# Kernel tuning notes

Hardware: AMD Instinct MI355X
Metric: run time of the kernel (lower is better)

## Reference

```python
import jax, jax.numpy as jnp
import numpy as np

N, E, G = 100000, 1600000, 2000
D_IN, D_H, D_MLP, D_OUT = 768, 128, 32, 2


def setup_inputs() -> dict:
    key = jax.random.key(0)
    ks = jax.random.split(key, 12)
    x = jax.random.normal(ks[0], (N, D_IN), dtype=jnp.float32)
    edge_index = jax.random.randint(ks[1], (2, E), 0, N, dtype=jnp.int64)
    edge_attr = jax.random.uniform(ks[2], (E, 1), dtype=jnp.float32)
    batch = jnp.sort(jax.random.randint(ks[3], (N,), 0, G, dtype=jnp.int64))
    s1 = 1.0 / np.sqrt(D_IN)
    s2 = 1.0 / np.sqrt(D_H)
    s3 = 1.0 / np.sqrt(D_MLP)
    return {
        "x": x, "edge_index": edge_index, "edge_attr": edge_attr,
        "batch": batch, "num_graphs": G,
        "W1i": jax.random.normal(ks[4], (D_IN, D_H), dtype=jnp.float32) * s1,
        "W1r": jax.random.normal(ks[5], (D_IN, D_H), dtype=jnp.float32) * s1,
        "b1": jnp.zeros((D_H,), dtype=jnp.float32),
        "W2i": jax.random.normal(ks[6], (D_H, D_H), dtype=jnp.float32) * s2,
        "W2r": jax.random.normal(ks[7], (D_H, D_H), dtype=jnp.float32) * s2,
        "b2": jnp.zeros((D_H,), dtype=jnp.float32),
        "Wl1": jax.random.normal(ks[8], (D_H, D_MLP), dtype=jnp.float32) * s2,
        "bl1": jnp.zeros((D_MLP,), dtype=jnp.float32),
        "Wl2": jax.random.normal(ks[9], (D_MLP, D_OUT), dtype=jnp.float32) * s3,
        "bl2": jnp.zeros((D_OUT,), dtype=jnp.float32),
    }


def _arma_conv(x, row, col, ew, Wi, Wr, b, n_nodes):
    # gcn_norm without self-loops: D^{-1/2} A D^{-1/2}
    deg = jax.ops.segment_sum(ew, col, num_segments=n_nodes)
    dinv = jnp.where(deg > 0, jax.lax.rsqrt(jnp.where(deg > 0, deg, 1.0)), 0.0)
    norm = dinv[row] * ew * dinv[col]
    h = x @ Wi                                   # [N, F_out]
    msg = h[row] * norm[:, None]                 # gather + scale  [E, F_out]
    agg = jax.ops.segment_sum(msg, col, num_segments=n_nodes)
    return jax.nn.relu(agg + x @ Wr + b)         # ARMA: K=1, T=1, act=ReLU


def reference(x, edge_index, edge_attr, batch, num_graphs,
              W1i, W1r, b1, W2i, W2r, b2, Wl1, bl1, Wl2, bl2):
    row, col = edge_index[0], edge_index[1]
    ew = edge_attr.reshape(-1)
    n = x.shape[0]
    h = jax.nn.elu(_arma_conv(x, row, col, ew, W1i, W1r, b1, n))
    node_x = _arma_conv(h, row, col, ew, W2i, W2r, b2, n)
    # global mean pool over graphs
    sums = jax.ops.segment_sum(node_x, batch, num_segments=num_graphs)
    cnt = jax.ops.segment_sum(jnp.ones((n,), node_x.dtype), batch, num_segments=num_graphs)
    graph_x = sums / jnp.maximum(cnt, 1.0)[:, None]
    pred = jax.nn.elu(graph_x @ Wl1 + bl1) @ Wl2 + bl2
    return pred
```

## Files before the change

### kernel.cpp

```cpp
#include <hip/hip_runtime.h>
#include <hip/hip_bf16.h>
#include <math.h>

typedef __attribute__((ext_vector_type(8))) short short8;
typedef __attribute__((ext_vector_type(4))) float f32x4;
typedef __attribute__((ext_vector_type(2))) float f32x2;
typedef __attribute__((address_space(1))) const void gvoid;
typedef __attribute__((address_space(3))) void lvoid;

#define NC 8

__device__ __forceinline__ unsigned short f2bf(float f) {
    unsigned int u = __builtin_bit_cast(unsigned int, f);
    return (unsigned short)((u + 0x7fffu + ((u >> 16) & 1u)) >> 16);
}
__device__ __forceinline__ float b2f(short s) {
    return __builtin_bit_cast(float, ((unsigned int)(unsigned short)s) << 16);
}
__device__ __forceinline__ unsigned int cvtpk(float lo, float hi) {
    unsigned int r;
    asm("v_cvt_pk_bf16_f32 %0, %1, %2" : "=v"(r) : "v"(lo), "v"(hi));
    return r;
}
__device__ __forceinline__ unsigned int pk8_lo(float a, float b, unsigned int old) {
    return (unsigned int)__builtin_amdgcn_cvt_pk_fp8_f32(a, b, (int)old, false);
}
__device__ __forceinline__ unsigned int pk8_hi(float a, float b, unsigned int old) {
    return (unsigned int)__builtin_amdgcn_cvt_pk_fp8_f32(a, b, (int)old, true);
}
__device__ __forceinline__ f32x2 up8_lo(unsigned int v) {
    return __builtin_amdgcn_cvt_pk_f32_fp8((int)v, false);
}
__device__ __forceinline__ f32x2 up8_hi(unsigned int v) {
    return __builtin_amdgcn_cvt_pk_f32_fp8((int)v, true);
}
__device__ __forceinline__ void acc16(float* A, const uint4 u, const float n) {
    f32x2 p;
    p = up8_lo(u.x); A[0]  = fmaf(p.x, n, A[0]);  A[1]  = fmaf(p.y, n, A[1]);
    p = up8_hi(u.x); A[2]  = fmaf(p.x, n, A[2]);  A[3]  = fmaf(p.y, n, A[3]);
    p = up8_lo(u.y); A[4]  = fmaf(p.x, n, A[4]);  A[5]  = fmaf(p.y, n, A[5]);
    p = up8_hi(u.y); A[6]  = fmaf(p.x, n, A[6]);  A[7]  = fmaf(p.y, n, A[7]);
    p = up8_lo(u.z); A[8]  = fmaf(p.x, n, A[8]);  A[9]  = fmaf(p.y, n, A[9]);
    p = up8_hi(u.z); A[10] = fmaf(p.x, n, A[10]); A[11] = fmaf(p.y, n, A[11]);
    p = up8_lo(u.w); A[12] = fmaf(p.x, n, A[12]); A[13] = fmaf(p.y, n, A[13]);
    p = up8_hi(u.w); A[14] = fmaf(p.x, n, A[14]); A[15] = fmaf(p.y, n, A[15]);
}

__global__ __launch_bounds__(256) void hist_conv_kernel(
    const int* __restrict__ ei, const float* __restrict__ ea,
    unsigned long long* __restrict__ packed, int* __restrict__ rank, int N, int E,
    int eBlocks,
    const float* __restrict__ W1i, const float* __restrict__ W1r,
    const float* __restrict__ W2i, const float* __restrict__ W2r,
    unsigned short* __restrict__ W1t, unsigned short* __restrict__ W2t)
{
    if ((int)blockIdx.x < eBlocks) {
        int e = blockIdx.x * 256 + threadIdx.x;
        if (e >= E) return;
        const int copy = blockIdx.x & (NC - 1);
        int c = ei[(size_t)E + e];
        unsigned long long fx = (unsigned long long)(ea[e] * 1048576.0f + 0.5f);
        unsigned long long old = atomicAdd(&packed[(size_t)copy * N + c], (1ULL << 42) | fx);
        rank[e] = (int)(old >> 42);
    } else {
        int id = (blockIdx.x - eBlocks) * 256 + threadIdx.x;
        if (id < 256 * 768) {
            int n = id / 768, j = id % 768;
            int k = (j & ~63) | ((((j >> 3) & 7) ^ (n & 7)) << 3) | (j & 7);
            float v = (n < 128) ? W1i[k * 128 + n] : W1r[k * 128 + (n - 128)];
            W1t[id] = f2bf(v);
        } else {
            int id2 = id - 256 * 768;
            if (id2 < 128 * 256) {
                int n = id2 >> 8, j = id2 & 255;
                int k = (j & ~63) | ((((j >> 3) & 7) ^ (n & 7)) << 3) | (j & 7);
                float v = (k < 128) ? W2i[k * 128 + n] : W2r[(k - 128) * 128 + n];
                W2t[id2] = f2bf(v);
            }
        }
    }
}

__global__ __launch_bounds__(256) void scan1p_kernel(
    const unsigned long long* __restrict__ packed, int* __restrict__ out,
    int* __restrict__ blksum, int n)
{
    __shared__ int part[256];
    const int t = threadIdx.x;
    const int base = blockIdx.x * 1024 + t * 4;
    int v[4];
#pragma unroll
    for (int q = 0; q < 4; ++q) {
        int s = 0;
        if (base + q < n) {
#pragma unroll
            for (int p = 0; p < NC; ++p)
                s += (int)(packed[(size_t)p * n + base + q] >> 42);
        }
        v[q] = s;
    }
    const int s = v[0] + v[1] + v[2] + v[3];
    part[t] = s;
    __syncthreads();
    for (int off = 1; off < 256; off <<= 1) {
        int x = (t >= off) ? part[t - off] : 0;
        __syncthreads();
        part[t] += x;
        __syncthreads();
    }
    if (t == 255) blksum[blockIdx.x] = part[255];
    int run = part[t] - s;
#pragma unroll
    for (int q = 0; q < 4; ++q) {
        if (base + q < n) out[base + q] = run;
        run += v[q];
    }
}

__global__ __launch_bounds__(256) void scan3_kernel(
    int* __restrict__ rowptr, const int* __restrict__ blksum,
    int* __restrict__ wpb, const unsigned long long* __restrict__ packed,
    float* __restrict__ dinv, int n, int Etot, int nb)
{
    __shared__ int tmp[256];
    __shared__ int sexcl[256];
    const int t = threadIdx.x;
    const int v = (t < nb) ? blksum[t] : 0;
    tmp[t] = v;
    __syncthreads();
    for (int off = 1; off < 256; off <<= 1) {
        int x = (t >= off) ? tmp[t - off] : 0;
        __syncthreads();
        tmp[t] += x;
        __syncthreads();
    }
    sexcl[t] = tmp[t] - v;
    __syncthreads();
    const int i = blockIdx.x * 256 + t;
    if (i == 0) rowptr[n] = Etot;
    if (i >= n) return;
    int base = rowptr[i] + sexcl[i >> 10];
    rowptr[i] = base;
    unsigned long long degfx = 0;
    int acc = base;
#pragma unroll
    for (int p = 0; p < NC; ++p) {
        unsigned long long vv = packed[(size_t)p * n + i];
        wpb[(size_t)p * n + i] = acc;
        acc += (int)(vv >> 42);
        degfx += vv & ((1ULL << 42) - 1);
    }
    dinv[i] = (degfx > 0) ? rsqrtf((float)degfx * 9.5367431640625e-7f) : 0.f;
}

__global__ __launch_bounds__(512) void gemm1_place_kernel(
    const float* __restrict__ A, const unsigned short* __restrict__ Wt,
    const float* __restrict__ bias, unsigned char* __restrict__ outP8,
    unsigned short* __restrict__ outR, int M, int K, int gB,
    const int* __restrict__ ei, const float* __restrict__ ea,
    const float* __restrict__ dinv, const int* __restrict__ wpb,
    const int* __restrict__ rank, int2* __restrict__ csr, int E)
{
    __shared__ __align__(16) unsigned char As[2][64 * 128];
    __shared__ __align__(16) unsigned char Bs[256 * 128];

    if ((int)blockIdx.x >= gB) {
        int e = (blockIdx.x - gB) * 512 + threadIdx.x;
        if (e >= E) return;
        const int copy = (e >> 8) & (NC - 1);
        int r = ei[e];
        int c = ei[(size_t)E + e];
        float nm = dinv[r] * ea[e] * dinv[c];
        int pos = wpb[(size_t)copy * M + c] + rank[e];
        int2 rec;
        rec.x = r;
        rec.y = __builtin_bit_cast(int, nm);
        csr[pos] = rec;
        return;
    }

    const int t = threadIdx.x;
    const int m0 = blockIdx.x * 64;
    const int lane = t & 63;
    const int wid = t >> 6;
    const int wm = wid >> 2;
    const int wn = wid & 3;
    const int lr = lane & 15;
    const int lk = (lane >> 4) * 8;

    f32x4 acc[2][4] = {};

    const int sr = t >> 3;
    const int sk = (t & 7) * 8;
    const int aRow = m0 + sr;
    const bool aOk = (aRow < M);
    const float* aSrc = A + (size_t)(aOk ? aRow : 0) * K + sk;
    const int aDst = sr * 128 + ((sk * 2) ^ ((sr & 7) << 4));
    const unsigned short* bSrc = Wt + (size_t)(lane >> 3) * K + (lane & 7) * 8;

    const int NIT = K >> 6;

#pragma unroll
    for (int i = 0; i < 4; ++i) {
        const int chunk = i * 8 + wid;
        __builtin_amdgcn_global_load_lds(
            (gvoid*)(bSrc + (size_t)chunk * 8 * K),
            (lvoid*)(Bs + chunk * 1024), 16, 0, 0);
    }
    {
        float4 f0 = {}, f1 = {};
        if (aOk) { f0 = *(const float4*)(aSrc); f1 = *(const float4*)(aSrc + 4); }
        uint4 uv = {cvtpk(f0.x, f0.y), cvtpk(f0.z, f0.w),
                    cvtpk(f1.x, f1.y), cvtpk(f1.z, f1.w)};
        *(uint4*)(&As[0][aDst]) = uv;
    }

    for (int it = 0; it < NIT; ++it) {
        const int cur = it & 1;
        const int nxt = cur ^ 1;
        const bool hasNext = (it + 1 < NIT);
        const int k1 = (it + 1) << 6;

        __syncthreads();

        float4 g0 = {}, g1 = {};
        if (hasNext && aOk) {
            g0 = *(const float4*)(aSrc + k1);
            g1 = *(const float4*)(aSrc + k1 + 4);
        }

#pragma unroll
        for (int ks = 0; ks < 2; ++ks) {
            short8 a[2], b[4];
#pragma unroll
            for (int mf = 0; mf < 2; ++mf) {
                const int r = wm * 32 + mf * 16 + lr;
                a[mf] = *(const short8*)(&As[cur][r * 128 + (((ks * 32 + lk) * 2) ^ ((r & 7) << 4))]);
            }
#pragma unroll
            for (int nf = 0; nf < 4; ++nf) {
                const int n = wn * 64 + nf * 16 + lr;
                b[nf] = *(const short8*)(Bs + n * 128 + (((ks * 32 + lk) * 2) ^ ((n & 7) << 4)));
            }
#pragma unroll
            for (int mf = 0; mf < 2; ++mf)
#pragma unroll
                for (int nf = 0; nf < 4; ++nf)
                    acc[mf][nf] = __builtin_amdgcn_mfma_f32_16x16x32_bf16(
                        a[mf], b[nf], acc[mf][nf], 0, 0, 0);
        }

        if (hasNext) {
            uint4 uv = {cvtpk(g0.x, g0.y), cvtpk(g0.z, g0.w),
                        cvtpk(g1.x, g1.y), cvtpk(g1.z, g1.w)};
            *(uint4*)(&As[nxt][aDst]) = uv;
        }

        __syncthreads();

        if (hasNext) {
#pragma unroll
            for (int i = 0; i < 4; ++i) {
                const int chunk = i * 8 + wid;
                __builtin_amdgcn_global_load_lds(
                    (gvoid*)(bSrc + (size_t)chunk * 8 * K + k1),
                    (lvoid*)(Bs + chunk * 1024), 16, 0, 0);
            }
        }
    }

#pragma unroll
    for (int mf = 0; mf < 2; ++mf) {
#pragma unroll
        for (int nf = 0; nf < 4; ++nf) {
            const int n = wn * 64 + nf * 16 + lr;
            const f32x4 v = acc[mf][nf];
            const int mb = m0 + wm * 32 + mf * 16 + (lane >> 4) * 4;
            if (n < 128) {
                const unsigned int u01 = pk8_lo(v[0], v[1], 0u);
                const unsigned int u23 = pk8_lo(v[2], v[3], 0u);
                if (mb + 0 < M) outP8[(size_t)(mb + 0) * 128 + n] = (unsigned char)(u01);
                if (mb + 1 < M) outP8[(size_t)(mb + 1) * 128 + n] = (unsigned char)(u01 >> 8);
                if (mb + 2 < M) outP8[(size_t)(mb + 2) * 128 + n] = (unsigned char)(u23);
                if (mb + 3 < M) outP8[(size_t)(mb + 3) * 128 + n] = (unsigned char)(u23 >> 8);
            } else {
                const int nl = n - 128;
                const float badd = bias[nl];
#pragma unroll
                for (int j = 0; j < 4; ++j) {
                    if (mb + j < M) outR[(size_t)(mb + j) * 128 + nl] = f2bf(v[j] + badd);
                }
            }
        }
    }
}

__global__ __launch_bounds__(512) void gemm_mfma_single(
    const unsigned short* __restrict__ Aa,
    const unsigned short* __restrict__ Ah,
    const unsigned short* __restrict__ Wt,
    const float* __restrict__ bias,
    unsigned short* __restrict__ outX, int M)
{
    __shared__ __align__(16) unsigned char As[128 * 128];
    __shared__ __align__(16) unsigned char Bs[128 * 128];

    const int t = threadIdx.x;
    const int m0 = blockIdx.x * 128;
    const int lane = t & 63;
    const int wid = t >> 6;
    const int wm = wid >> 1;
    const int wn = wid & 1;
    const int lr = lane & 15;
    const int lk = (lane >> 4) * 8;

    f32x4 acc[2][4] = {};

    const int sr = t >> 2;
    const int sk = (t & 3) * 16;
    const int aRow = m0 + sr;
    const bool aOk = (aRow < M);
    const int rowSafe = aOk ? aRow : 0;
    const int sw = (sr & 7) << 4;
    const unsigned short* bSrc = Wt + (size_t)(lane >> 3) * 256 + (lane & 7) * 8;

    for (int k0 = 0; k0 < 256; k0 += 64) {
#pragma unroll
        for (int i = 0; i < 2; ++i) {
            const int chunk = i * 8 + wid;
            __builtin_amdgcn_global_load_lds(
                (gvoid*)(bSrc + (size_t)chunk * 8 * 256 + k0),
                (lvoid*)(Bs + chunk * 1024), 16, 0, 0);
        }
        const unsigned short* src =
            (k0 < 128 ? Aa : Ah) + (size_t)rowSafe * 128 + (k0 & 127) + sk;
        const short8 v0 = *(const short8*)(src);
        const short8 v1 = *(const short8*)(src + 8);
        *(short8*)(As + sr * 128 + ((sk * 2) ^ sw)) = v0;
        *(short8*)(As + sr * 128 + ((sk * 2 + 16) ^ sw)) = v1;
        __syncthreads();
#pragma unroll
        for (int ks = 0; ks < 2; ++ks) {
            short8 a[2], b[4];
#pragma unroll
            for (int mf = 0; mf < 2; ++mf) {
                const int r = wm * 32 + mf * 16 + lr;
                a[mf] = *(const short8*)(As + r * 128 + (((ks * 32 + lk) * 2) ^ ((r & 7) << 4)));
            }
#pragma unroll
            for (int nf = 0; nf < 4; ++nf) {
                const int n = wn * 64 + nf * 16 + lr;
                b[nf] = *(const short8*)(Bs + n * 128 + (((ks * 32 + lk) * 2) ^ ((n & 7) << 4)));
            }
#pragma unroll
            for (int mf = 0; mf < 2; ++mf)
#pragma unroll
                for (int nf = 0; nf < 4; ++nf)
                    acc[mf][nf] = __builtin_amdgcn_mfma_f32_16x16x32_bf16(
                        a[mf], b[nf], acc[mf][nf], 0, 0, 0);
        }
        __syncthreads();
    }

#pragma unroll
    for (int mf = 0; mf < 2; ++mf) {
#pragma unroll
        for (int nf = 0; nf < 4; ++nf) {
            const int n = wn * 64 + nf * 16 + lr;
            const float bb = bias[n];
            const f32x4 v = acc[mf][nf];
#pragma unroll
            for (int j = 0; j < 4; ++j) {
                const int m = m0 + wm * 32 + mf * 16 + (lane >> 4) * 4 + j;
                if (m < M) outX[(size_t)m * 128 + n] = f2bf(fmaxf(v[j] + bb, 0.f));
            }
        }
    }
}

__global__ __launch_bounds__(256) void agg_bias_relu(
    const unsigned char* __restrict__ P8, const unsigned short* __restrict__ Rbf,
    const int* __restrict__ rowptr, const int2* __restrict__ csr,
    unsigned short* __restrict__ hout, unsigned char* __restrict__ h8out, int N)
{
    const int i = blockIdx.x * 32 + (threadIdx.x >> 3);
    const int l = threadIdx.x & 7;
    if (i >= N) return;
    const int beg = rowptr[i];
    const int end = rowptr[i + 1];
    const int c = l * 16;

    float A0[16] = {}, A1[16] = {};
    int j = beg;
    for (; j + 1 < end; j += 2) {
        const int2 e0 = csr[j], e1 = csr[j + 1];
        const uint4 u0 = *(const uint4*)(P8 + (size_t)e0.x * 128 + c);
        const uint4 u1 = *(const uint4*)(P8 + (size_t)e1.x * 128 + c);
        acc16(A0, u0, __builtin_bit_cast(float, e0.y));
        acc16(A1, u1, __builtin_bit_cast(float, e1.y));
    }
    if (j < end) {
        const int2 e0 = csr[j];
        const uint4 u0 = *(const uint4*)(P8 + (size_t)e0.x * 128 + c);
        acc16(A0, u0, __builtin_bit_cast(float, e0.y));
    }
    const short8 r0 = *(const short8*)(Rbf + (size_t)i * 128 + c);
    const short8 r1 = *(const short8*)(Rbf + (size_t)i * 128 + c + 8);
    float s[16];
    short8 o0, o1;
#pragma unroll
    for (int q = 0; q < 8; ++q) {
        s[q] = fmaxf(A0[q] + A1[q] + b2f(r0[q]), 0.f);
        o0[q] = (short)f2bf(s[q]);
    }
#pragma unroll
    for (int q = 8; q < 16; ++q) {
        s[q] = fmaxf(A0[q] + A1[q] + b2f(r1[q - 8]), 0.f);
        o1[q - 8] = (short)f2bf(s[q]);
    }
    *(short8*)(hout + (size_t)i * 128 + c) = o0;
    *(short8*)(hout + (size_t)i * 128 + c + 8) = o1;
    uint4 w;
    w.x = pk8_hi(s[2],  s[3],  pk8_lo(s[0],  s[1],  0u));
    w.y = pk8_hi(s[6],  s[7],  pk8_lo(s[4],  s[5],  0u));
    w.z = pk8_hi(s[10], s[11], pk8_lo(s[8],  s[9],  0u));
    w.w = pk8_hi(s[14], s[15], pk8_lo(s[12], s[13], 0u));
    *(uint4*)(h8out + (size_t)i * 128 + c) = w;
}

__global__ __launch_bounds__(256) void agg_plain(
    const unsigned char* __restrict__ H8,
    const int* __restrict__ rowptr, const int2* __restrict__ csr,
    unsigned short* __restrict__ ahout, int N)
{
    const int i = blockIdx.x * 32 + (threadIdx.x >> 3);
    const int l = threadIdx.x & 7;
    if (i >= N) return;
    const int beg = rowptr[i];
    const int end = rowptr[i + 1];
    const int c = l * 16;

    float A0[16] = {}, A1[16] = {};
    int j = beg;
    for (; j + 1 < end; j += 2) {
        const int2 e0 = csr[j], e1 = csr[j + 1];
        const uint4 u0 = *(const uint4*)(H8 + (size_t)e0.x * 128 + c);
        const uint4 u1 = *(const uint4*)(H8 + (size_t)e1.x * 128 + c);
        acc16(A0, u0, __builtin_bit_cast(float, e0.y));
        acc16(A1, u1, __builtin_bit_cast(float, e1.y));
    }
    if (j < end) {
        const int2 e0 = csr[j];
        const uint4 u0 = *(const uint4*)(H8 + (size_t)e0.x * 128 + c);
        acc16(A0, u0, __builtin_bit_cast(float, e0.y));
    }
    short8 o0, o1;
#pragma unroll
    for (int q = 0; q < 8; ++q)  o0[q] = (short)f2bf(A0[q] + A1[q]);
#pragma unroll
    for (int q = 8; q < 16; ++q) o1[q - 8] = (short)f2bf(A0[q] + A1[q]);
    *(short8*)(ahout + (size_t)i * 128 + c) = o0;
    *(short8*)(ahout + (size_t)i * 128 + c + 8) = o1;
}

__global__ __launch_bounds__(256) void pool_mlp(
    const unsigned short* __restrict__ nx, const int* __restrict__ batch, int N,
    const float* __restrict__ Wl1, const float* __restrict__ bl1,
    const float* __restrict__ Wl2, const float* __restrict__ bl2,
    float* __restrict__ out)
{
    __shared__ float gxp[4][128];
    __shared__ float hid[32];
    __shared__ int rng[2];
    const int g = blockIdx.x;
    const int t = threadIdx.x;
    if (t < 2) {
        const int target = g + t;
        int lo = 0, hi = N;
        while (lo < hi) {
            int mid = (lo + hi) >> 1;
            if (batch[mid] < target) lo = mid + 1; else hi = mid;
        }
        rng[t] = lo;
    }
    __syncthreads();
    const int s = rng[0], e = rng[1];
    const int pr = t & 63;
    const int strm = t >> 6;
    float a0 = 0.f, b0 = 0.f, a1 = 0.f, b1 = 0.f;
    int i = s + strm;
    for (; i + 4 < e; i += 8) {
        const unsigned int u = *(const unsigned int*)&nx[(size_t)i * 128 + pr * 2];
        const unsigned int v = *(const unsigned int*)&nx[(size_t)(i + 4) * 128 + pr * 2];
        a0 += b2f((short)(u & 0xffff)); b0 += b2f((short)(u >> 16));
        a1 += b2f((short)(v & 0xffff)); b1 += b2f((short)(v >> 16));
    }
    if (i < e) {
        const unsigned int u = *(const unsigned int*)&nx[(size_t)i * 128 + pr * 2];
        a0 += b2f((short)(u & 0xffff)); b0 += b2f((short)(u >> 16));
    }
    gxp[strm][pr * 2] = a0 + a1;
    gxp[strm][pr * 2 + 1] = b0 + b1;
    __syncthreads();
    if (t < 128) {
        gxp[0][t] = ((gxp[0][t] + gxp[1][t]) + (gxp[2][t] + gxp[3][t]))
                    / fmaxf((float)(e - s), 1.f);
    }
    __syncthreads();
    if (t < 32) {
        float a = bl1[t];
#pragma unroll 8
        for (int k = 0; k < 128; ++k) a = fmaf(gxp[0][k], Wl1[k * 32 + t], a);
        hid[t] = a > 0.f ? a : expm1f(a);
    }
    __syncthreads();
    if (t < 2) {
        float a = bl2[t];
#pragma unroll
        for (int k = 0; k < 32; ++k) a = fmaf(hid[k], Wl2[k * 2 + t], a);
        out[(size_t)g * 2 + t] = a;
    }
}

extern "C" void kernel_launch(void* const* d_in, const int* in_sizes, int n_in,
                              void* d_out, int out_size, void* d_ws, size_t ws_size,
                              hipStream_t stream)
{
    const float* x     = (const float*)d_in[0];
    const int*   ei    = (const int*)d_in[1];
    const float* ea    = (const float*)d_in[2];
    const int*   batch = (const int*)d_in[3];
    const float* W1i   = (const float*)d_in[5];
    const float* W1r   = (const float*)d_in[6];
    const float* b1    = (const float*)d_in[7];
    const float* W2i   = (const float*)d_in[8];
    const float* W2r   = (const float*)d_in[9];
    const float* b2    = (const float*)d_in[10];
    const float* Wl1   = (const float*)d_in[11];
    const float* bl1   = (const float*)d_in[12];
    const float* Wl2   = (const float*)d_in[13];
    const float* bl2   = (const float*)d_in[14];

    const int N = in_sizes[0] / 768;
    const int E = in_sizes[2];
    const int G = out_size / 2;

    char* ws = (char*)d_ws;
    size_t off = 0;
    auto alloc = [&](size_t bytes) -> char* {
        char* p = ws + off;
        off = (off + bytes + 255) & ~(size_t)255;
        return p;
    };
    unsigned long long* packed = (unsigned long long*)alloc((size_t)NC * N * 8);
    int*   rank    = (int*)alloc((size_t)E * 4);
    int*   wpb     = (int*)alloc((size_t)NC * N * 4);
    float* dinv    = (float*)alloc((size_t)N * 4);
    int*   rowptr  = (int*)alloc((size_t)(N + 1) * 4);
    int*   blksum  = (int*)alloc((size_t)256 * 4);
    int2*  csr     = (int2*)alloc((size_t)E * 8);
    unsigned char*  P8   = (unsigned char*)alloc((size_t)N * 128);
    unsigned char*  H8   = (unsigned char*)alloc((size_t)N * 128);
    unsigned short* R1   = (unsigned short*)alloc((size_t)N * 128 * 2);
    unsigned short* hbf  = (unsigned short*)alloc((size_t)N * 128 * 2);
    unsigned short* ahb  = (unsigned short*)alloc((size_t)N * 128 * 2);
    unsigned short* nxb  = (unsigned short*)alloc((size_t)N * 128 * 2);
    unsigned short* W1t  = (unsigned short*)alloc((size_t)256 * 768 * 2);
    unsigned short* W2t  = (unsigned short*)alloc((size_t)128 * 256 * 2);

    const int eBlocks = (E + 255) / 256;
    const int cBlocks = (256 * 768 + 128 * 256 + 255) / 256;
    const int nb      = (N + 1023) / 1024;
    const int nBlocks = (N + 255) / 256;
    const int aBlocks = (N + 31) / 32;
    const int gB      = (N + 63) / 64;
    const int pB      = (E + 511) / 512;

    (void)hipMemsetAsync(packed, 0, (size_t)NC * N * 8, stream);
    hist_conv_kernel<<<eBlocks + cBlocks, 256, 0, stream>>>(
        ei, ea, packed, rank, N, E, eBlocks, W1i, W1r, W2i, W2r, W1t, W2t);
    scan1p_kernel<<<nb, 256, 0, stream>>>(packed, rowptr, blksum, N);
    scan3_kernel<<<nBlocks, 256, 0, stream>>>(rowptr, blksum, wpb, packed, dinv, N, E, nb);

    gemm1_place_kernel<<<gB + pB, 512, 0, stream>>>(
        x, W1t, b1, P8, R1, N, 768, gB, ei, ea, dinv, wpb, rank, csr, E);

    agg_bias_relu<<<aBlocks, 256, 0, stream>>>(P8, R1, rowptr, csr, hbf, H8, N);

    agg_plain<<<aBlocks, 256, 0, stream>>>(H8, rowptr, csr, ahb, N);
    gemm_mfma_single<<<(N + 127) / 128, 512, 0, stream>>>(ahb, hbf, W2t, b2, nxb, N);

    pool_mlp<<<G, 256, 0, stream>>>(nxb, batch, N, Wl1, bl1, Wl2, bl2, (float*)d_out);
}
```

Before: 374.7 us.

## Pre-convert x to tiled swizzled bf16 and stream A tiles via global_load_lds

The fp32 input x is now converted to bf16 inside the first histogram kernel and written in a per-block tiled, pre-swizzled layout. The first GEMM then loads A tiles straight into LDS with global_load_lds, dropping the register-staged fp32 loads, conversions and the A double buffer. This costs an extra pass over x: a 307MB read plus a 154MB bf16 write and reread, where before x was read once inside the GEMM. The GEMM also loses its A-tile double buffering.

```diff
diff --git a/kernel.cpp b/kernel.cpp
--- a/kernel.cpp
+++ b/kernel.cpp
@@ -49,21 +49,23 @@
 __global__ __launch_bounds__(256) void hist_conv_kernel(
     const int* __restrict__ ei, const float* __restrict__ ea,
     unsigned long long* __restrict__ packed, int* __restrict__ rank, int N, int E,
-    int eBlocks,
+    int eBlocks, int cBlocks,
     const float* __restrict__ W1i, const float* __restrict__ W1r,
     const float* __restrict__ W2i, const float* __restrict__ W2r,
-    unsigned short* __restrict__ W1t, unsigned short* __restrict__ W2t)
-{
-    if ((int)blockIdx.x < eBlocks) {
-        int e = blockIdx.x * 256 + threadIdx.x;
+    unsigned short* __restrict__ W1t, unsigned short* __restrict__ W2t,
+    const float* __restrict__ X, uint4* __restrict__ Xbf)
+{
+    const int bid = (int)blockIdx.x;
+    if (bid < eBlocks) {
+        int e = bid * 256 + threadIdx.x;
         if (e >= E) return;
-        const int copy = blockIdx.x & (NC - 1);
+        const int copy = bid & (NC - 1);
         int c = ei[(size_t)E + e];
         unsigned long long fx = (unsigned long long)(ea[e] * 1048576.0f + 0.5f);
         unsigned long long old = atomicAdd(&packed[(size_t)copy * N + c], (1ULL << 42) | fx);
         rank[e] = (int)(old >> 42);
-    } else {
-        int id = (blockIdx.x - eBlocks) * 256 + threadIdx.x;
+    } else if (bid < eBlocks + cBlocks) {
+        int id = (bid - eBlocks) * 256 + threadIdx.x;
         if (id < 256 * 768) {
             int n = id / 768, j = id % 768;
             int k = (j & ~63) | ((((j >> 3) & 7) ^ (n & 7)) << 3) | (j & 7);
@@ -78,6 +80,25 @@
                 W2t[id2] = f2bf(v);
             }
         }
+    } else {
+        const int rb = bid - eBlocks - cBlocks;
+        const int row0 = rb * 64;
+        for (int i = threadIdx.x; i < 64 * 96; i += 256) {
+            const int row = i / 96;
+            const int gk  = i - row * 96;
+            const int kb  = gk >> 3;
+            const int gs  = gk & 7;
+            const int gd  = gs ^ (row & 7);
+            uint4 uv = {0u, 0u, 0u, 0u};
+            if (row0 + row < N) {
+                const float* src = X + (size_t)(row0 + row) * 768 + kb * 64 + gs * 8;
+                const float4 f0 = *(const float4*)src;
+                const float4 f1 = *(const float4*)(src + 4);
+                uv.x = cvtpk(f0.x, f0.y); uv.y = cvtpk(f0.z, f0.w);
+                uv.z = cvtpk(f1.x, f1.y); uv.w = cvtpk(f1.z, f1.w);
+            }
+            Xbf[(size_t)(rb * 12 + kb) * 512 + row * 8 + gd] = uv;
+        }
     }
 }
 
@@ -154,14 +175,14 @@
 }
 
 __global__ __launch_bounds__(512) void gemm1_place_kernel(
-    const float* __restrict__ A, const unsigned short* __restrict__ Wt,
+    const uint4* __restrict__ Xbf, const unsigned short* __restrict__ Wt,
     const float* __restrict__ bias, unsigned char* __restrict__ outP8,
     unsigned short* __restrict__ outR, int M, int K, int gB,
     const int* __restrict__ ei, const float* __restrict__ ea,
     const float* __restrict__ dinv, const int* __restrict__ wpb,
     const int* __restrict__ rank, int2* __restrict__ csr, int E)
 {
-    __shared__ __align__(16) unsigned char As[2][64 * 128];
+    __shared__ __align__(16) unsigned char As[64 * 128];
     __shared__ __align__(16) unsigned char Bs[256 * 128];
 
     if ((int)blockIdx.x >= gB) {
@@ -190,16 +211,13 @@
 
     f32x4 acc[2][4] = {};
 
-    const int sr = t >> 3;
-    const int sk = (t & 7) * 8;
-    const int aRow = m0 + sr;
-    const bool aOk = (aRow < M);
-    const float* aSrc = A + (size_t)(aOk ? aRow : 0) * K + sk;
-    const int aDst = sr * 128 + ((sk * 2) ^ ((sr & 7) << 4));
+    const int NIT = K >> 6;
+    const unsigned char* aSrc =
+        (const unsigned char*)Xbf + (size_t)blockIdx.x * NIT * 8192 + (size_t)t * 16;
+    unsigned char* aDst = As + (t >> 6) * 1024;
     const unsigned short* bSrc = Wt + (size_t)(lane >> 3) * K + (lane & 7) * 8;
 
-    const int NIT = K >> 6;
-
+    __builtin_amdgcn_global_load_lds((gvoid*)aSrc, (lvoid*)aDst, 16, 0, 0);
 #pragma unroll
     for (int i = 0; i < 4; ++i) {
         const int chunk = i * 8 + wid;
@@ -207,35 +225,17 @@
             (gvoid*)(bSrc + (size_t)chunk * 8 * K),
             (lvoid*)(Bs + chunk * 1024), 16, 0, 0);
     }
-    {
-        float4 f0 = {}, f1 = {};
-        if (aOk) { f0 = *(const float4*)(aSrc); f1 = *(const float4*)(aSrc + 4); }
-        uint4 uv = {cvtpk(f0.x, f0.y), cvtpk(f0.z, f0.w),
-                    cvtpk(f1.x, f1.y), cvtpk(f1.z, f1.w)};
-        *(uint4*)(&As[0][aDst]) = uv;
-    }
 
     for (int it = 0; it < NIT; ++it) {
-        const int cur = it & 1;
-        const int nxt = cur ^ 1;
-        const bool hasNext = (it + 1 < NIT);
         const int k1 = (it + 1) << 6;
-
-        __syncthreads();
-
-        float4 g0 = {}, g1 = {};
-        if (hasNext && aOk) {
-            g0 = *(const float4*)(aSrc + k1);
-            g1 = *(const float4*)(aSrc + k1 + 4);
-        }
-
+        __syncthreads();
 #pragma unroll
         for (int ks = 0; ks < 2; ++ks) {
             short8 a[2], b[4];
 #pragma unroll
             for (int mf = 0; mf < 2; ++mf) {
                 const int r = wm * 32 + mf * 16 + lr;
-                a[mf] = *(const short8*)(&As[cur][r * 128 + (((ks * 32 + lk) * 2) ^ ((r & 7) << 4))]);
+                a[mf] = *(const short8*)(As + r * 128 + (((ks * 32 + lk) * 2) ^ ((r & 7) << 4)));
             }
 #pragma unroll
             for (int nf = 0; nf < 4; ++nf) {
@@ -249,16 +249,10 @@
                     acc[mf][nf] = __builtin_amdgcn_mfma_f32_16x16x32_bf16(
                         a[mf], b[nf], acc[mf][nf], 0, 0, 0);
         }
-
-        if (hasNext) {
-            uint4 uv = {cvtpk(g0.x, g0.y), cvtpk(g0.z, g0.w),
-                        cvtpk(g1.x, g1.y), cvtpk(g1.z, g1.w)};
-            *(uint4*)(&As[nxt][aDst]) = uv;
-        }
-
-        __syncthreads();
-
-        if (hasNext) {
+        __syncthreads();
+        if (it + 1 < NIT) {
+            __builtin_amdgcn_global_load_lds(
+                (gvoid*)(aSrc + (size_t)(it + 1) * 8192), (lvoid*)aDst, 16, 0, 0);
 #pragma unroll
             for (int i = 0; i < 4; ++i) {
                 const int chunk = i * 8 + wid;
@@ -552,6 +546,7 @@
         off = (off + bytes + 255) & ~(size_t)255;
         return p;
     };
+    const int gB = (N + 63) / 64;
     unsigned long long* packed = (unsigned long long*)alloc((size_t)NC * N * 8);
     int*   rank    = (int*)alloc((size_t)E * 4);
     int*   wpb     = (int*)alloc((size_t)NC * N * 4);
@@ -559,6 +554,7 @@
     int*   rowptr  = (int*)alloc((size_t)(N + 1) * 4);
     int*   blksum  = (int*)alloc((size_t)256 * 4);
     int2*  csr     = (int2*)alloc((size_t)E * 8);
+    uint4* Xbf     = (uint4*)alloc((size_t)gB * 12 * 8192);
     unsigned char*  P8   = (unsigned char*)alloc((size_t)N * 128);
     unsigned char*  H8   = (unsigned char*)alloc((size_t)N * 128);
     unsigned short* R1   = (unsigned short*)alloc((size_t)N * 128 * 2);
@@ -573,17 +569,17 @@
     const int nb      = (N + 1023) / 1024;
     const int nBlocks = (N + 255) / 256;
     const int aBlocks = (N + 31) / 32;
-    const int gB      = (N + 63) / 64;
     const int pB      = (E + 511) / 512;
 
     (void)hipMemsetAsync(packed, 0, (size_t)NC * N * 8, stream);
-    hist_conv_kernel<<<eBlocks + cBlocks, 256, 0, stream>>>(
-        ei, ea, packed, rank, N, E, eBlocks, W1i, W1r, W2i, W2r, W1t, W2t);
+    hist_conv_kernel<<<eBlocks + cBlocks + gB, 256, 0, stream>>>(
+        ei, ea, packed, rank, N, E, eBlocks, cBlocks,
+        W1i, W1r, W2i, W2r, W1t, W2t, x, Xbf);
     scan1p_kernel<<<nb, 256, 0, stream>>>(packed, rowptr, blksum, N);
     scan3_kernel<<<nBlocks, 256, 0, stream>>>(rowptr, blksum, wpb, packed, dinv, N, E, nb);
 
     gemm1_place_kernel<<<gB + pB, 512, 0, stream>>>(
-        x, W1t, b1, P8, R1, N, 768, gB, ei, ea, dinv, wpb, rank, csr, E);
+        Xbf, W1t, b1, P8, R1, N, 768, gB, ei, ea, dinv, wpb, rank, csr, E);
 
     agg_bias_relu<<<aBlocks, 256, 0, stream>>>(P8, R1, rowptr, csr, hbf, H8, N);
 
```

Measured after the change: 445.3 us. +18.9%, slower.

## Stage whole 32-row A panel into LDS upfront in gemm1, halve M tile

Applied to the files above, without the earlier changes.

The first GEMM's M tile drops from 64 to 32 rows per block. Each block now loads its full 32x768 fp32 A panel once, converts it to bf16 and stores it in LDS as 12 K-slices, replacing the per-iteration double-buffered A loads. The goal is to issue all A global loads at once for more memory-level parallelism and to remove per-step A conversion from the K loop. In exchange, each B tile is now reused across only 32 rows, so W traffic doubles and more blocks are launched, and the larger LDS footprint may limit occupancy.

```diff
diff --git a/kernel.cpp b/kernel.cpp
--- a/kernel.cpp
+++ b/kernel.cpp
@@ -161,7 +161,7 @@
     const float* __restrict__ dinv, const int* __restrict__ wpb,
     const int* __restrict__ rank, int2* __restrict__ csr, int E)
 {
-    __shared__ __align__(16) unsigned char As[2][64 * 128];
+    __shared__ __align__(16) unsigned char As[12][32 * 128];
     __shared__ __align__(16) unsigned char Bs[256 * 128];
 
     if ((int)blockIdx.x >= gB) {
@@ -180,7 +180,7 @@
     }
 
     const int t = threadIdx.x;
-    const int m0 = blockIdx.x * 64;
+    const int m0 = blockIdx.x * 32;
     const int lane = t & 63;
     const int wid = t >> 6;
     const int wm = wid >> 2;
@@ -188,18 +188,31 @@
     const int lr = lane & 15;
     const int lk = (lane >> 4) * 8;
 
-    f32x4 acc[2][4] = {};
-
-    const int sr = t >> 3;
-    const int sk = (t & 7) * 8;
-    const int aRow = m0 + sr;
-    const bool aOk = (aRow < M);
-    const float* aSrc = A + (size_t)(aOk ? aRow : 0) * K + sk;
-    const int aDst = sr * 128 + ((sk * 2) ^ ((sr & 7) << 4));
+    f32x4 acc[4] = {};
+
+    {
+        const int pr  = t >> 4;
+        const int seg = t & 15;
+        const int aRow = m0 + pr;
+        const bool aOk = (aRow < M);
+        const float* aSrc = A + (size_t)(aOk ? aRow : 0) * K + seg * 48;
+        const int swz = (pr & 7) << 4;
+#pragma unroll
+        for (int j = 0; j < 6; ++j) {
+            float4 f0 = {}, f1 = {};
+            if (aOk) {
+                f0 = *(const float4*)(aSrc + j * 8);
+                f1 = *(const float4*)(aSrc + j * 8 + 4);
+            }
+            uint4 uv = {cvtpk(f0.x, f0.y), cvtpk(f0.z, f0.w),
+                        cvtpk(f1.x, f1.y), cvtpk(f1.z, f1.w)};
+            const int G = seg * 6 + j;
+            const int kt = G >> 3;
+            const int g  = G & 7;
+            *(uint4*)(&As[kt][pr * 128 + ((g * 16) ^ swz)]) = uv;
+        }
+    }
     const unsigned short* bSrc = Wt + (size_t)(lane >> 3) * K + (lane & 7) * 8;
-
-    const int NIT = K >> 6;
-
 #pragma unroll
     for (int i = 0; i < 4; ++i) {
         const int chunk = i * 8 + wid;
@@ -207,35 +220,15 @@
             (gvoid*)(bSrc + (size_t)chunk * 8 * K),
             (lvoid*)(Bs + chunk * 1024), 16, 0, 0);
     }
-    {
-        float4 f0 = {}, f1 = {};
-        if (aOk) { f0 = *(const float4*)(aSrc); f1 = *(const float4*)(aSrc + 4); }
-        uint4 uv = {cvtpk(f0.x, f0.y), cvtpk(f0.z, f0.w),
-                    cvtpk(f1.x, f1.y), cvtpk(f1.z, f1.w)};
-        *(uint4*)(&As[0][aDst]) = uv;
-    }
-
-    for (int it = 0; it < NIT; ++it) {
-        const int cur = it & 1;
-        const int nxt = cur ^ 1;
-        const bool hasNext = (it + 1 < NIT);
-        const int k1 = (it + 1) << 6;
-
-        __syncthreads();
-
-        float4 g0 = {}, g1 = {};
-        if (hasNext && aOk) {
-            g0 = *(const float4*)(aSrc + k1);
-            g1 = *(const float4*)(aSrc + k1 + 4);
-        }
-
+
+    for (int kt = 0; kt < 12; ++kt) {
+        __syncthreads();
 #pragma unroll
         for (int ks = 0; ks < 2; ++ks) {
-            short8 a[2], b[4];
-#pragma unroll
-            for (int mf = 0; mf < 2; ++mf) {
-                const int r = wm * 32 + mf * 16 + lr;
-                a[mf] = *(const short8*)(&As[cur][r * 128 + (((ks * 32 + lk) * 2) ^ ((r & 7) << 4))]);
+            short8 a, b[4];
+            {
+                const int r = wm * 16 + lr;
+                a = *(const short8*)(&As[kt][r * 128 + (((ks * 32 + lk) * 2) ^ ((r & 7) << 4))]);
             }
 #pragma unroll
             for (int nf = 0; nf < 4; ++nf) {
@@ -243,22 +236,12 @@
                 b[nf] = *(const short8*)(Bs + n * 128 + (((ks * 32 + lk) * 2) ^ ((n & 7) << 4)));
             }
 #pragma unroll
-            for (int mf = 0; mf < 2; ++mf)
-#pragma unroll
-                for (int nf = 0; nf < 4; ++nf)
-                    acc[mf][nf] = __builtin_amdgcn_mfma_f32_16x16x32_bf16(
-                        a[mf], b[nf], acc[mf][nf], 0, 0, 0);
-        }
-
-        if (hasNext) {
-            uint4 uv = {cvtpk(g0.x, g0.y), cvtpk(g0.z, g0.w),
-                        cvtpk(g1.x, g1.y), cvtpk(g1.z, g1.w)};
-            *(uint4*)(&As[nxt][aDst]) = uv;
-        }
-
-        __syncthreads();
-
-        if (hasNext) {
+            for (int nf = 0; nf < 4; ++nf)
+                acc[nf] = __builtin_amdgcn_mfma_f32_16x16x32_bf16(a, b[nf], acc[nf], 0, 0, 0);
+        }
+        __syncthreads();
+        if (kt + 1 < 12) {
+            const int k1 = (kt + 1) * 64;
 #pragma unroll
             for (int i = 0; i < 4; ++i) {
                 const int chunk = i * 8 + wid;
@@ -270,26 +253,23 @@
     }
 
 #pragma unroll
-    for (int mf = 0; mf < 2; ++mf) {
-#pragma unroll
-        for (int nf = 0; nf < 4; ++nf) {
-            const int n = wn * 64 + nf * 16 + lr;
-            const f32x4 v = acc[mf][nf];
-            const int mb = m0 + wm * 32 + mf * 16 + (lane >> 4) * 4;
-            if (n < 128) {
-                const unsigned int u01 = pk8_lo(v[0], v[1], 0u);
-                const unsigned int u23 = pk8_lo(v[2], v[3], 0u);
-                if (mb + 0 < M) outP8[(size_t)(mb + 0) * 128 + n] = (unsigned char)(u01);
-                if (mb + 1 < M) outP8[(size_t)(mb + 1) * 128 + n] = (unsigned char)(u01 >> 8);
-                if (mb + 2 < M) outP8[(size_t)(mb + 2) * 128 + n] = (unsigned char)(u23);
-                if (mb + 3 < M) outP8[(size_t)(mb + 3) * 128 + n] = (unsigned char)(u23 >> 8);
-            } else {
-                const int nl = n - 128;
-                const float badd = bias[nl];
-#pragma unroll
-                for (int j = 0; j < 4; ++j) {
-                    if (mb + j < M) outR[(size_t)(mb + j) * 128 + nl] = f2bf(v[j] + badd);
-                }
+    for (int nf = 0; nf < 4; ++nf) {
+        const int n = wn * 64 + nf * 16 + lr;
+        const f32x4 v = acc[nf];
+        const int mb = m0 + wm * 16 + (lane >> 4) * 4;
+        if (n < 128) {
+            const unsigned int u01 = pk8_lo(v[0], v[1], 0u);
+            const unsigned int u23 = pk8_lo(v[2], v[3], 0u);
+            if (mb + 0 < M) outP8[(size_t)(mb + 0) * 128 + n] = (unsigned char)(u01);
+            if (mb + 1 < M) outP8[(size_t)(mb + 1) * 128 + n] = (unsigned char)(u01 >> 8);
+            if (mb + 2 < M) outP8[(size_t)(mb + 2) * 128 + n] = (unsigned char)(u23);
+            if (mb + 3 < M) outP8[(size_t)(mb + 3) * 128 + n] = (unsigned char)(u23 >> 8);
+        } else {
+            const int nl = n - 128;
+            const float badd = bias[nl];
+#pragma unroll
+            for (int j = 0; j < 4; ++j) {
+                if (mb + j < M) outR[(size_t)(mb + j) * 128 + nl] = f2bf(v[j] + badd);
             }
         }
     }
@@ -573,7 +553,7 @@
     const int nb      = (N + 1023) / 1024;
     const int nBlocks = (N + 255) / 256;
     const int aBlocks = (N + 31) / 32;
-    const int gB      = (N + 63) / 64;
+    const int gB      = (N + 31) / 32;
     const int pB      = (E + 511) / 512;
 
     (void)hipMemsetAsync(packed, 0, (size_t)NC * N * 8, stream);
```

Result: slower. 421.1 us (+12.4%).
